# Optimization experiments

Hardware: AMD Instinct MI355X
Metric: run time of the kernel (lower is better)

Reference implementation:

```python
import jax, jax.numpy as jnp
import numpy as np

T = 8192   # sequence length (sent_len)
D = 512    # word_emb_dim
H = 2048   # enc_lstm_dim
S = 512    # number of segments (len(action_pos))
EPS = 1e-4 # additive constant in the original _masked_softmax denominator


def setup_inputs() -> dict:
    key = jax.random.key(0)
    ks = jax.random.split(key, 16)
    s = 0.02  # small init scale keeps exp() stable
    seg_len = T // S
    action_pos = (jnp.arange(1, S + 1, dtype=jnp.int32) * seg_len - 1)  # last = T-1
    action = jnp.zeros((T,), jnp.int32).at[action_pos].set(1)
    return {
        "sent": jax.random.normal(ks[0], (T, D), jnp.float32),
        "Wi1": jax.random.normal(ks[1], (3 * H, D), jnp.float32) * s,
        "Wh1": jax.random.normal(ks[2], (3 * H, H), jnp.float32) * s,
        "bi1": jax.random.normal(ks[3], (3 * H,), jnp.float32) * s,
        "bh1": jax.random.normal(ks[4], (3 * H,), jnp.float32) * s,
        "Wi2": jax.random.normal(ks[5], (3 * H, H), jnp.float32) * s,
        "Wh2": jax.random.normal(ks[6], (3 * H, H), jnp.float32) * s,
        "bi2": jax.random.normal(ks[7], (3 * H,), jnp.float32) * s,
        "bh2": jax.random.normal(ks[8], (3 * H,), jnp.float32) * s,
        "Wl": jax.random.normal(ks[9], (H, H), jnp.float32) * s,
        "bl": jax.random.normal(ks[10], (H,), jnp.float32) * s,
        "wa": jax.random.normal(ks[11], (H,), jnp.float32) * s,
        "Wl2": jax.random.normal(ks[12], (H, H), jnp.float32) * s,
        "bl2": jax.random.normal(ks[13], (H,), jnp.float32) * s,
        "wa2": jax.random.normal(ks[14], (H,), jnp.float32) * s,
        "action": action,
        "action_pos": action_pos,
    }


def _gru_scan(xs, reset, Wi, Wh, bi, bh):
    """GRU over leading axis; hidden state zeroed after steps where reset==1.
    xs: (N, in), reset: (N,) int. Returns outputs (N, H)."""
    gi_all = xs @ Wi.T + bi  # (N, 3H) precompute input gates as one GEMM

    def step(h, inp):
        gi, a = inp
        gh = Wh @ h + bh
        r = jax.nn.sigmoid(gi[:H] + gh[:H])
        z = jax.nn.sigmoid(gi[H:2 * H] + gh[H:2 * H])
        n = jnp.tanh(gi[2 * H:] + r * gh[2 * H:])
        hn = (1.0 - z) * n + z * h
        h_next = jnp.where(a == 1, jnp.zeros_like(hn), hn)
        return h_next, hn

    h0 = jnp.zeros((H,), xs.dtype)
    _, outs = jax.lax.scan(step, h0, (gi_all, reset))
    return outs


def _degenerate_softmax(a):
    # Original sums exp over a size-1 axis: w = exp(a) / (exp(a) + 1e-4)
    e = jnp.exp(a)
    return e / (e + EPS)


def reference(sent, Wi1, Wh1, bi1, bh1, Wi2, Wh2, bi2, bh2,
              Wl, bl, wa, Wl2, bl2, wa2, action, action_pos):
    # lower GRU with per-step state reset
    outs = _gru_scan(sent, action, Wi1, Wh1, bi1, bh1)          # (T, H)
    emb_h = jnp.tanh(outs @ Wl.T + bl)                           # (T, H)
    w = _degenerate_softmax(emb_h @ wa)                          # (T,)
    weighted = w[:, None] * emb_h                                # (T, H)
    # segment i covers tokens (action_pos[i-1], action_pos[i]]
    seg_id = jnp.searchsorted(action_pos, jnp.arange(T), side='left')
    seg = jax.ops.segment_max(weighted, seg_id, num_segments=S)  # (S, H)
    # upper GRU over segment embeddings (no resets, zero init)
    outs2 = _gru_scan(seg, jnp.zeros((S,), jnp.int32), Wi2, Wh2, bi2, bh2)
    e2 = jnp.tanh(outs2 @ Wl2.T + bl2)                           # (S, H)
    w2 = _degenerate_softmax(e2 @ wa2)                           # (S,)
    emb = jnp.max(w2[:, None] * e2, axis=0, keepdims=True)       # (1, H)
    return emb
```

## Files before the change

kernel.cpp:

```cpp
#include <hip/hip_runtime.h>
#include <stdint.h>

typedef unsigned short u16;
typedef unsigned int u32;
typedef unsigned long long u64;
typedef __attribute__((ext_vector_type(4))) float f32x4;
typedef __attribute__((ext_vector_type(8))) short bf16x8;
typedef __attribute__((ext_vector_type(4))) u32 u32x4;

constexpr int kT = 8192;
constexpr int kD = 512;
constexpr int kH = 2048;
constexpr int kH3 = 6144;
constexpr int kS = 512;
constexpr int kSeg = 16;
constexpr int kNWG2 = 256;
constexpr int kREP = 4;

__device__ __forceinline__ float bf2f(u16 u) {
  union { float f; u32 u; } v; v.u = ((u32)u) << 16; return v.f;
}
__device__ __forceinline__ u16 f2bf(float f) {
  union { float f; u32 u; } v; v.f = f;
  u32 lsb = (v.u >> 16) & 1u;
  v.u += 0x7fffu + lsb;
  return (u16)(v.u >> 16);
}
__device__ __forceinline__ float bflo(u32 x) {
  union { float f; u32 u; } v; v.u = x << 16; return v.f;
}
__device__ __forceinline__ float bfhi(u32 x) {
  union { float f; u32 u; } v; v.u = x & 0xffff0000u; return v.f;
}
__device__ __forceinline__ float sigm(float x) { return 1.f / (1.f + expf(-x)); }

__device__ __forceinline__ void g2l16(const u16* g, u16* l) {
  __builtin_amdgcn_global_load_lds(
      (const __attribute__((address_space(1))) u32*)g,
      (__attribute__((address_space(3))) u32*)l, 16, 0, 0);
}

__device__ __forceinline__ u32x4 bypass_load16(const u32* p) {
  u32x4 v;
  asm volatile("global_load_dwordx4 %0, %1, off sc0 sc1\n\ts_waitcnt vmcnt(0)"
               : "=&v"(v) : "v"(p) : "memory");
  return v;
}
__device__ __forceinline__ void bypass_store16(u32* p, u32x4 v) {
  asm volatile("global_store_dwordx4 %0, %1, off sc0 sc1" :: "v"(p), "v"(v) : "memory");
}

__global__ void cvt_bf16(const float* __restrict__ in, u16* __restrict__ out, int n4) {
  int i = blockIdx.x * blockDim.x + threadIdx.x;
  if (i >= n4) return;
  const float4 v = *(const float4*)(in + (size_t)i * 4);
  uint2 o;
  o.x = (u32)f2bf(v.x) | ((u32)f2bf(v.y) << 16);
  o.y = (u32)f2bf(v.z) | ((u32)f2bf(v.w) << 16);
  *(uint2*)(out + (size_t)i * 4) = o;
}

template<int EPI>
__global__ __launch_bounds__(256)
void gemm_bt(const u16* __restrict__ A, int lda,
             const u16* __restrict__ B, int ldb,
             u16* __restrict__ Obf, const float* __restrict__ bias,
             int M, int N, int K)
{
  __shared__ u16 ls[4 * 16384];
  const int tid = threadIdx.x;
  const int w = tid >> 6, lane = tid & 63;
  const int wr = w >> 1, wc = w & 1;
  const int arow0 = blockIdx.y * 128;
  const int brow0 = blockIdx.x * 128;
  const int srow = w * 32 + (lane >> 3);
  const int scol = (lane & 7) * 8;
  const u16* gA = A + (size_t)(arow0 + srow) * lda + scol;
  const u16* gB = B + (size_t)(brow0 + srow) * ldb + scol;
  const int sb = w * 32 * 64;

  f32x4 acc[4][4];
#pragma unroll
  for (int m = 0; m < 4; ++m)
#pragma unroll
    for (int n = 0; n < 4; ++n) acc[m][n] = (f32x4)0.f;

  const int fr = lane & 15;
  const int kq = lane >> 4;
  const int nk = K >> 6;

  auto stage = [&](int buf, int kt) {
    u16* la = &ls[buf * 16384 + sb];
    u16* lb = &ls[buf * 16384 + 8192 + sb];
#pragma unroll
    for (int i = 0; i < 4; ++i) g2l16(gA + (size_t)i * 8 * lda + kt, la + i * 8 * 64);
#pragma unroll
    for (int i = 0; i < 4; ++i) g2l16(gB + (size_t)i * 8 * ldb + kt, lb + i * 8 * 64);
  };

  stage(0, 0);
  if (nk > 1) stage(1, 64);
  if (nk > 2) stage(2, 128);

  for (int i = 0; i < nk; ++i) {
    if (i + 2 < nk) asm volatile("s_waitcnt vmcnt(16)" ::: "memory");
    else            asm volatile("s_waitcnt vmcnt(0)" ::: "memory");
    __builtin_amdgcn_s_barrier();
    __builtin_amdgcn_sched_barrier(0);
    if (i + 3 < nk) stage((i + 3) & 3, (i + 3) * 64);
    const u16* lsA = &ls[(i & 3) * 16384];
    const u16* lsB = lsA + 8192;
#pragma unroll
    for (int kk = 0; kk < 2; ++kk) {
      bf16x8 af[4], bq[4];
#pragma unroll
      for (int m = 0; m < 4; ++m)
        af[m] = *(const bf16x8*)&lsA[(wr * 64 + m * 16 + fr) * 64 + kk * 32 + kq * 8];
#pragma unroll
      for (int n = 0; n < 4; ++n)
        bq[n] = *(const bf16x8*)&lsB[(wc * 64 + n * 16 + fr) * 64 + kk * 32 + kq * 8];
#pragma unroll
      for (int m = 0; m < 4; ++m)
#pragma unroll
        for (int n = 0; n < 4; ++n)
          acc[m][n] = __builtin_amdgcn_mfma_f32_16x16x32_bf16(af[m], bq[n], acc[m][n], 0, 0, 0);
    }
  }

#pragma unroll
  for (int m = 0; m < 4; ++m) {
#pragma unroll
    for (int n = 0; n < 4; ++n) {
      const int row0 = arow0 + wr * 64 + m * 16 + kq * 4;
      const int col = brow0 + wc * 64 + n * 16 + fr;
      if (EPI == 1) {
#pragma unroll
        for (int i = 0; i < 4; ++i)
          Obf[(size_t)(row0 + i) * N + col] = f2bf(acc[m][n][i]);
      } else {
        const float bv = bias[col];
#pragma unroll
        for (int i = 0; i < 4; ++i)
          Obf[(size_t)(row0 + i) * N + col] = f2bf(tanhf(acc[m][n][i] + bv));
      }
    }
  }
}

__global__ __launch_bounds__(256) void gru1_gates(
    const u32* __restrict__ gi32, int segStride, const u16* __restrict__ gh,
    const float* __restrict__ bi, const float* __restrict__ bh,
    u16* __restrict__ h_bf, u16* __restrict__ outs_bf, int t, int ghvalid)
{
  const int idx = blockIdx.x * 256 + threadIdx.x;
  const int seg = idx >> 10, jp = idx & 1023;
  const u32* gh32 = (const u32*)gh;
  const int gbase = seg * segStride;
  const int base = seg * 3072;
  const u32 gir = gi32[gbase + jp];
  const u32 giz = gi32[gbase + 1024 + jp];
  const u32 gin = gi32[gbase + 2048 + jp];
  u32 ghr = 0, ghz = 0, ghn = 0, hp = 0;
  if (ghvalid) {
    ghr = gh32[base + jp];
    ghz = gh32[base + 1024 + jp];
    ghn = gh32[base + 2048 + jp];
    hp = ((const u32*)h_bf)[seg * 1024 + jp];
  }
  const float2 bir = *(const float2*)&bi[2 * jp];
  const float2 biz = *(const float2*)&bi[kH + 2 * jp];
  const float2 bin = *(const float2*)&bi[2 * kH + 2 * jp];
  const float2 bhr = *(const float2*)&bh[2 * jp];
  const float2 bhz = *(const float2*)&bh[kH + 2 * jp];
  const float2 bhn = *(const float2*)&bh[2 * kH + 2 * jp];
  float hn[2];
#pragma unroll
  for (int e = 0; e < 2; ++e) {
    const float gr = e ? bfhi(gir) : bflo(gir), hr = e ? bfhi(ghr) : bflo(ghr);
    const float gz = e ? bfhi(giz) : bflo(giz), hz = e ? bfhi(ghz) : bflo(ghz);
    const float gn = e ? bfhi(gin) : bflo(gin), hh = e ? bfhi(ghn) : bflo(ghn);
    const float r = sigm(gr + (e ? bir.y : bir.x) + hr + (e ? bhr.y : bhr.x));
    const float z = sigm(gz + (e ? biz.y : biz.x) + hz + (e ? bhz.y : bhz.x));
    const float n = tanhf(gn + (e ? bin.y : bin.x) + r * (hh + (e ? bhn.y : bhn.x)));
    const float hprev = e ? bfhi(hp) : bflo(hp);
    hn[e] = (1.f - z) * n + z * hprev;
  }
  const u32 packed = (u32)f2bf(hn[0]) | ((u32)f2bf(hn[1]) << 16);
  ((u32*)h_bf)[seg * 1024 + jp] = packed;
  ((u32*)outs_bf)[(size_t)(seg * kSeg + t) * 1024 + jp] = packed;
}

__global__ __launch_bounds__(256) void seg_weight_max(
    const u16* __restrict__ embh, const float* __restrict__ wa,
    u16* __restrict__ seg_bf)
{
  __shared__ float wrow[16];
  const int s = blockIdx.x, tid = threadIdx.x;
  const int w = tid >> 6, lane = tid & 63;
#pragma unroll
  for (int rr = 0; rr < 4; ++rr) {
    const int r = w * 4 + rr;
    const u16* row = embh + ((size_t)s * kSeg + r) * kH;
    float p = 0.f;
#pragma unroll
    for (int k = 0; k < 32; ++k) {
      const int c = lane + 64 * k;
      p += bf2f(row[c]) * wa[c];
    }
#pragma unroll
    for (int off = 32; off; off >>= 1) p += __shfl_down(p, off, 64);
    if (lane == 0) { const float e = expf(p); wrow[r] = e / (e + 1e-4f); }
  }
  __syncthreads();
#pragma unroll
  for (int i = 0; i < 8; ++i) {
    const int c = tid + 256 * i;
    float m = -1e30f;
#pragma unroll
    for (int r = 0; r < 16; ++r)
      m = fmaxf(m, wrow[r] * bf2f(embh[((size_t)s * kSeg + r) * kH + c]));
    seg_bf[(size_t)s * kH + c] = f2bf(m);
  }
}

__global__ __launch_bounds__(512)
void gru2_persistent(const u16* __restrict__ Wh2bf, const u16* __restrict__ gi2b,
                     const float* __restrict__ bi2, const float* __restrict__ bh2,
                     u32* __restrict__ hx,
                     u16* __restrict__ outs2)
{
  __shared__ u32 hlb[2][1024];
  __shared__ float gil_all[512 * 24];
  __shared__ float rowsum[24];
  __shared__ u16 hnl[8];
  const int wg = blockIdx.x, tid = threadIdx.x;
  const int g0 = wg * 8;
  const int rep = wg & (kREP - 1);
  const int w = tid >> 6, lane = tid & 63;

  u32 w0[16], w1[16], w2r[16];
#pragma unroll
  for (int rr = 0; rr < 3; ++rr) {
    const int lr = w * 3 + rr;
    const int grow = (lr >> 3) * kH + g0 + (lr & 7);
    const u32* src = (const u32*)(Wh2bf + (size_t)grow * kH) + lane * 16;
#pragma unroll
    for (int i = 0; i < 16; ++i) {
      const u32 val = src[i];
      if (rr == 0) w0[i] = val;
      else if (rr == 1) w1[i] = val;
      else w2r[i] = val;
    }
  }
  for (int i = tid; i < 512 * 24; i += 512) {
    const int t = i / 24, idx = i - t * 24;
    gil_all[i] = bf2f(gi2b[(size_t)t * kH3 + (idx >> 3) * kH + g0 + (idx & 7)]);
  }
  float bir = 0, biz = 0, bin = 0, bhr = 0, bhz = 0, bhn = 0;
  if (tid < 8) {
    const int jj = g0 + tid;
    bir = bi2[jj]; biz = bi2[kH + jj]; bin = bi2[2 * kH + jj];
    bhr = bh2[jj]; bhz = bh2[kH + jj]; bhn = bh2[2 * kH + jj];
  }

  for (int t = 0; t < 512; ++t) {
    const int par = t & 1;
    const u32 want = (u32)t & 0xffffu;
    const u32* p = hx + ((size_t)par * kREP + rep) * 2048 + 4 * tid;
    u32x4 v = bypass_load16(p);
    for (;;) {
      const u32 bad = ((v.x ^ want) | (v.y ^ want) | (v.z ^ want) | (v.w ^ want)) & 0xffffu;
      if (!__any((int)bad)) break;
      if (bad) v = bypass_load16(p);
    }
    hlb[par][2 * tid]     = (v.x >> 16) | (v.y & 0xffff0000u);
    hlb[par][2 * tid + 1] = (v.z >> 16) | (v.w & 0xffff0000u);
    __syncthreads();
    const uint4* hp4 = (const uint4*)&hlb[par][0];
    float hf[32];
#pragma unroll
    for (int q = 0; q < 4; ++q) {
      const uint4 hv = hp4[lane * 4 + q];
      hf[8 * q + 0] = bflo(hv.x); hf[8 * q + 1] = bfhi(hv.x);
      hf[8 * q + 2] = bflo(hv.y); hf[8 * q + 3] = bfhi(hv.y);
      hf[8 * q + 4] = bflo(hv.z); hf[8 * q + 5] = bfhi(hv.z);
      hf[8 * q + 6] = bflo(hv.w); hf[8 * q + 7] = bfhi(hv.w);
    }
    float a0 = 0.f, a1 = 0.f, a2 = 0.f;
#pragma unroll
    for (int i = 0; i < 16; ++i) {
      a0 += bflo(w0[i]) * hf[2 * i] + bfhi(w0[i]) * hf[2 * i + 1];
      a1 += bflo(w1[i]) * hf[2 * i] + bfhi(w1[i]) * hf[2 * i + 1];
      a2 += bflo(w2r[i]) * hf[2 * i] + bfhi(w2r[i]) * hf[2 * i + 1];
    }
#pragma unroll
    for (int off = 32; off; off >>= 1) {
      a0 += __shfl_down(a0, off, 64);
      a1 += __shfl_down(a1, off, 64);
      a2 += __shfl_down(a2, off, 64);
    }
    if (lane == 0) {
      rowsum[w * 3 + 0] = a0;
      rowsum[w * 3 + 1] = a1;
      rowsum[w * 3 + 2] = a2;
    }
    __syncthreads();
    if (tid < 8) {
      const float r = sigm(gil_all[t * 24 + tid] + bir + rowsum[tid] + bhr);
      const float z = sigm(gil_all[t * 24 + 8 + tid] + biz + rowsum[8 + tid] + bhz);
      const float n = tanhf(gil_all[t * 24 + 16 + tid] + bin +
                            r * (rowsum[16 + tid] + bhn));
      const u32 hw = hlb[par][(g0 + tid) >> 1];
      const float hprev = (tid & 1) ? bfhi(hw) : bflo(hw);
      hnl[tid] = f2bf((1.f - z) * n + z * hprev);
    }
    if (tid < 2 * kREP) {
      const int orep = tid >> 1, half = tid & 1;
      const u32 tagv = (u32)(t + 1) & 0xffffu;
      u32x4 m;
      m.x = ((u32)hnl[half * 4 + 0] << 16) | tagv;
      m.y = ((u32)hnl[half * 4 + 1] << 16) | tagv;
      m.z = ((u32)hnl[half * 4 + 2] << 16) | tagv;
      m.w = ((u32)hnl[half * 4 + 3] << 16) | tagv;
      u32* q = hx + ((size_t)(1 - par) * kREP + orep) * 2048 + wg * 8 + half * 4;
      bypass_store16(q, m);
    }
    if (tid == 0)
      *(uint4*)&outs2[(size_t)t * kH + g0] = *(const uint4*)hnl;
  }
}

__global__ void calc_w2(const u16* __restrict__ e2, const float* __restrict__ wa2,
                        float* __restrict__ w2) {
  const int s = blockIdx.x, lane = threadIdx.x;
  float p = 0.f;
#pragma unroll
  for (int k = 0; k < 32; ++k) {
    const int c = lane + 64 * k;
    p += bf2f(e2[(size_t)s * kH + c]) * wa2[c];
  }
#pragma unroll
  for (int off = 32; off; off >>= 1) p += __shfl_down(p, off, 64);
  if (lane == 0) { const float e = expf(p); w2[s] = e / (e + 1e-4f); }
}

__global__ void final_max(const u16* __restrict__ e2, const float* __restrict__ w2,
                          float* __restrict__ out) {
  const int j = blockIdx.x * blockDim.x + threadIdx.x;
  float m = -1e30f;
  for (int s = 0; s < 512; ++s)
    m = fmaxf(m, w2[s] * bf2f(e2[(size_t)s * kH + j]));
  out[j] = m;
}

extern "C" void kernel_launch(void* const* d_in, const int* in_sizes, int n_in,
                              void* d_out, int out_size, void* d_ws, size_t ws_size,
                              hipStream_t stream)
{
  (void)in_sizes; (void)n_in; (void)out_size;
  const float* sent = (const float*)d_in[0];
  const float* Wi1f = (const float*)d_in[1];
  const float* Wh1f = (const float*)d_in[2];
  const float* bi1  = (const float*)d_in[3];
  const float* bh1  = (const float*)d_in[4];
  const float* Wi2f = (const float*)d_in[5];
  const float* Wh2f = (const float*)d_in[6];
  const float* bi2  = (const float*)d_in[7];
  const float* bh2  = (const float*)d_in[8];
  const float* Wlf  = (const float*)d_in[9];
  const float* bl   = (const float*)d_in[10];
  const float* wa   = (const float*)d_in[11];
  const float* Wl2f = (const float*)d_in[12];
  const float* bl2  = (const float*)d_in[13];
  const float* wa2  = (const float*)d_in[14];
  float* out = (float*)d_out;

  char* base = (char*)d_ws;
  size_t off = 0;
  auto alloc = [&](size_t b) { char* p = base + off; off += (b + 255) & ~(size_t)255; return p; };
  u16* sent_bf = (u16*)alloc((size_t)kT * kD * 2);
  u16* Wi1b    = (u16*)alloc((size_t)kH3 * kD * 2);
  u16* Wh1b    = (u16*)alloc((size_t)kH3 * kH * 2);
  u16* Wi2b    = (u16*)alloc((size_t)kH3 * kH * 2);
  u16* Wh2b    = (u16*)alloc((size_t)kH3 * kH * 2);
  u16* Wlb     = (u16*)alloc((size_t)kH * kH * 2);
  u16* Wl2b    = (u16*)alloc((size_t)kH * kH * 2);
  u16* gi_buf  = (u16*)alloc((size_t)kS * kH3 * 2);
  u16* gh_buf  = (u16*)alloc((size_t)kS * kH3 * 2);
  u16* h1b     = (u16*)alloc((size_t)kS * kH * 2);
  u16* outs_bf = (u16*)alloc((size_t)kT * kH * 2);
  u16* seg_bf  = (u16*)alloc((size_t)kS * kH * 2);
  u32* hx      = (u32*)alloc((size_t)2 * kREP * 2048 * 4);
  u16* outs2   = (u16*)alloc((size_t)kS * kH * 2);
  u16* e2b     = (u16*)alloc((size_t)kS * kH * 2);
  float* w2    = (float*)alloc(kS * 4);
  const size_t off_before_gi = off;
  u16* gi_all  = (u16*)alloc((size_t)kT * kH3 * 2);
  const bool fused_gi = (off <= ws_size);
  if (!fused_gi) off = off_before_gi;
  u16* embh = sent_bf;
  u16* gi2b = gi_buf;

  (void)hipMemsetAsync(hx, 0, (size_t)2 * kREP * 2048 * 4, stream);

  auto cvt = [&](const float* src, u16* dst, int n) {
    const int n4 = n / 4;
    cvt_bf16<<<dim3((n4 + 255) / 256), dim3(256), 0, stream>>>(src, dst, n4);
  };
  cvt(sent, sent_bf, kT * kD);
  cvt(Wi1f, Wi1b, kH3 * kD);
  cvt(Wh1f, Wh1b, kH3 * kH);
  cvt(Wi2f, Wi2b, kH3 * kH);
  cvt(Wlf, Wlb, kH * kH);
  cvt(Wl2f, Wl2b, kH * kH);
  cvt(Wh2f, Wh2b, kH3 * kH);

  if (fused_gi) {
    gemm_bt<1><<<dim3(kH3 / 128, kT / 128), dim3(256), 0, stream>>>(
        sent_bf, kD, Wi1b, kD, gi_all, nullptr, kT, kH3, kD);
  }
  for (int t = 0; t < kSeg; ++t) {
    if (t > 0) {
      gemm_bt<1><<<dim3(kH3 / 128, kS / 128), dim3(256), 0, stream>>>(
          h1b, kH, Wh1b, kH, gh_buf, nullptr, kS, kH3, kH);
    }
    const u32* gi32;
    int segStride;
    if (fused_gi) {
      gi32 = (const u32*)gi_all + (size_t)t * 3072;
      segStride = kSeg * 3072;
    } else {
      gemm_bt<1><<<dim3(kH3 / 128, kS / 128), dim3(256), 0, stream>>>(
          sent_bf + t * kD, kSeg * kD, Wi1b, kD, gi_buf, nullptr, kS, kH3, kD);
      gi32 = (const u32*)gi_buf;
      segStride = 3072;
    }
    gru1_gates<<<dim3(kS * kH / 512), dim3(256), 0, stream>>>(
        gi32, segStride, gh_buf, bi1, bh1, h1b, outs_bf, t, t > 0 ? 1 : 0);
  }
  gemm_bt<2><<<dim3(kH / 128, kT / 128), dim3(256), 0, stream>>>(
      outs_bf, kH, Wlb, kH, embh, bl, kT, kH, kH);
  seg_weight_max<<<dim3(kS), dim3(256), 0, stream>>>(embh, wa, seg_bf);
  gemm_bt<1><<<dim3(kH3 / 128, kS / 128), dim3(256), 0, stream>>>(
      seg_bf, kH, Wi2b, kH, gi2b, nullptr, kS, kH3, kH);
  gru2_persistent<<<dim3(kNWG2), dim3(512), 0, stream>>>(
      Wh2b, gi2b, bi2, bh2, hx, outs2);
  gemm_bt<2><<<dim3(kH / 128, kS / 128), dim3(256), 0, stream>>>(
      outs2, kH, Wl2b, kH, e2b, bl2, kS, kH, kH);
  calc_w2<<<dim3(kS), dim3(64), 0, stream>>>(e2b, wa2, w2);
  final_max<<<dim3(kH / 256), dim3(256), 0, stream>>>(e2b, w2, out);
}
```

Measured before the change: 2.510 ms.

## Assign one hidden unit per wave in GRU2 step to drop second barrier

Reorganizes the persistent upper-GRU kernel so each wave owns all three gate rows (r, z, n) of one hidden unit instead of three arbitrary rows. Each wave can then reduce its own dot products and apply the gate math in lane 0 directly, removing the rowsum shared buffer and the second __syncthreads per timestep. Each lane 0 now publishes its own tagged hidden word with four scalar bypass stores to the replicas, replacing the 16-byte vector stores done by a few threads. The weight slices are also laid out so LDS reads of h are contiguous per lane. The trade-off is more, smaller global stores per step.

```diff
diff --git a/kernel.cpp b/kernel.cpp
--- a/kernel.cpp
+++ b/kernel.cpp
@@ -46,8 +46,8 @@
                : "=&v"(v) : "v"(p) : "memory");
   return v;
 }
-__device__ __forceinline__ void bypass_store16(u32* p, u32x4 v) {
-  asm volatile("global_store_dwordx4 %0, %1, off sc0 sc1" :: "v"(p), "v"(v) : "memory");
+__device__ __forceinline__ void bypass_store4(u32* p, u32 v) {
+  asm volatile("global_store_dword %0, %1, off sc0 sc1" :: "v"(p), "v"(v) : "memory");
 }
 
 __global__ void cvt_bf16(const float* __restrict__ in, u16* __restrict__ out, int n4) {
@@ -231,37 +231,33 @@
 {
   __shared__ u32 hlb[2][1024];
   __shared__ float gil_all[512 * 24];
-  __shared__ float rowsum[24];
-  __shared__ u16 hnl[8];
   const int wg = blockIdx.x, tid = threadIdx.x;
   const int g0 = wg * 8;
   const int rep = wg & (kREP - 1);
   const int w = tid >> 6, lane = tid & 63;
-
-  u32 w0[16], w1[16], w2r[16];
-#pragma unroll
-  for (int rr = 0; rr < 3; ++rr) {
-    const int lr = w * 3 + rr;
-    const int grow = (lr >> 3) * kH + g0 + (lr & 7);
-    const u32* src = (const u32*)(Wh2bf + (size_t)grow * kH) + lane * 16;
-#pragma unroll
-    for (int i = 0; i < 16; ++i) {
-      const u32 val = src[i];
-      if (rr == 0) w0[i] = val;
-      else if (rr == 1) w1[i] = val;
-      else w2r[i] = val;
-    }
+  const int jj = g0 + w;
+
+  u32 wr_[16], wz_[16], wn_[16];
+  {
+    const u32* rr = (const u32*)(Wh2bf + (size_t)jj * kH);
+    const u32* rz = (const u32*)(Wh2bf + (size_t)(kH + jj) * kH);
+    const u32* rn = (const u32*)(Wh2bf + (size_t)(2 * kH + jj) * kH);
+#pragma unroll
+    for (int q = 0; q < 4; ++q)
+#pragma unroll
+      for (int i = 0; i < 4; ++i) {
+        const int idx = q * 256 + lane * 4 + i;
+        wr_[q * 4 + i] = rr[idx];
+        wz_[q * 4 + i] = rz[idx];
+        wn_[q * 4 + i] = rn[idx];
+      }
   }
   for (int i = tid; i < 512 * 24; i += 512) {
     const int t = i / 24, idx = i - t * 24;
     gil_all[i] = bf2f(gi2b[(size_t)t * kH3 + (idx >> 3) * kH + g0 + (idx & 7)]);
   }
-  float bir = 0, biz = 0, bin = 0, bhr = 0, bhz = 0, bhn = 0;
-  if (tid < 8) {
-    const int jj = g0 + tid;
-    bir = bi2[jj]; biz = bi2[kH + jj]; bin = bi2[2 * kH + jj];
-    bhr = bh2[jj]; bhz = bh2[kH + jj]; bhn = bh2[2 * kH + jj];
-  }
+  const float bir = bi2[jj], biz = bi2[kH + jj], bin = bi2[2 * kH + jj];
+  const float bhr = bh2[jj], bhz = bh2[kH + jj], bhn = bh2[2 * kH + jj];
 
   for (int t = 0; t < 512; ++t) {
     const int par = t & 1;
@@ -277,56 +273,39 @@
     hlb[par][2 * tid + 1] = (v.z >> 16) | (v.w & 0xffff0000u);
     __syncthreads();
     const uint4* hp4 = (const uint4*)&hlb[par][0];
-    float hf[32];
+    float ar = 0.f, az = 0.f, an = 0.f;
 #pragma unroll
     for (int q = 0; q < 4; ++q) {
-      const uint4 hv = hp4[lane * 4 + q];
-      hf[8 * q + 0] = bflo(hv.x); hf[8 * q + 1] = bfhi(hv.x);
-      hf[8 * q + 2] = bflo(hv.y); hf[8 * q + 3] = bfhi(hv.y);
-      hf[8 * q + 4] = bflo(hv.z); hf[8 * q + 5] = bfhi(hv.z);
-      hf[8 * q + 6] = bflo(hv.w); hf[8 * q + 7] = bfhi(hv.w);
-    }
-    float a0 = 0.f, a1 = 0.f, a2 = 0.f;
-#pragma unroll
-    for (int i = 0; i < 16; ++i) {
-      a0 += bflo(w0[i]) * hf[2 * i] + bfhi(w0[i]) * hf[2 * i + 1];
-      a1 += bflo(w1[i]) * hf[2 * i] + bfhi(w1[i]) * hf[2 * i + 1];
-      a2 += bflo(w2r[i]) * hf[2 * i] + bfhi(w2r[i]) * hf[2 * i + 1];
+      const uint4 hv = hp4[q * 64 + lane];
+      const float hf[8] = { bflo(hv.x), bfhi(hv.x), bflo(hv.y), bfhi(hv.y),
+                            bflo(hv.z), bfhi(hv.z), bflo(hv.w), bfhi(hv.w) };
+#pragma unroll
+      for (int i = 0; i < 4; ++i) {
+        const u32 wrv = wr_[q * 4 + i], wzv = wz_[q * 4 + i], wnv = wn_[q * 4 + i];
+        ar += bflo(wrv) * hf[2 * i] + bfhi(wrv) * hf[2 * i + 1];
+        az += bflo(wzv) * hf[2 * i] + bfhi(wzv) * hf[2 * i + 1];
+        an += bflo(wnv) * hf[2 * i] + bfhi(wnv) * hf[2 * i + 1];
+      }
     }
 #pragma unroll
     for (int off = 32; off; off >>= 1) {
-      a0 += __shfl_down(a0, off, 64);
-      a1 += __shfl_down(a1, off, 64);
-      a2 += __shfl_down(a2, off, 64);
+      ar += __shfl_down(ar, off, 64);
+      az += __shfl_down(az, off, 64);
+      an += __shfl_down(an, off, 64);
     }
     if (lane == 0) {
-      rowsum[w * 3 + 0] = a0;
-      rowsum[w * 3 + 1] = a1;
-      rowsum[w * 3 + 2] = a2;
-    }
-    __syncthreads();
-    if (tid < 8) {
-      const float r = sigm(gil_all[t * 24 + tid] + bir + rowsum[tid] + bhr);
-      const float z = sigm(gil_all[t * 24 + 8 + tid] + biz + rowsum[8 + tid] + bhz);
-      const float n = tanhf(gil_all[t * 24 + 16 + tid] + bin +
-                            r * (rowsum[16 + tid] + bhn));
-      const u32 hw = hlb[par][(g0 + tid) >> 1];
-      const float hprev = (tid & 1) ? bfhi(hw) : bflo(hw);
-      hnl[tid] = f2bf((1.f - z) * n + z * hprev);
-    }
-    if (tid < 2 * kREP) {
-      const int orep = tid >> 1, half = tid & 1;
-      const u32 tagv = (u32)(t + 1) & 0xffffu;
-      u32x4 m;
-      m.x = ((u32)hnl[half * 4 + 0] << 16) | tagv;
-      m.y = ((u32)hnl[half * 4 + 1] << 16) | tagv;
-      m.z = ((u32)hnl[half * 4 + 2] << 16) | tagv;
-      m.w = ((u32)hnl[half * 4 + 3] << 16) | tagv;
-      u32* q = hx + ((size_t)(1 - par) * kREP + orep) * 2048 + wg * 8 + half * 4;
-      bypass_store16(q, m);
-    }
-    if (tid == 0)
-      *(uint4*)&outs2[(size_t)t * kH + g0] = *(const uint4*)hnl;
+      const float r = sigm(gil_all[t * 24 + w] + bir + ar + bhr);
+      const float z = sigm(gil_all[t * 24 + 8 + w] + biz + az + bhz);
+      const float n = tanhf(gil_all[t * 24 + 16 + w] + bin + r * (an + bhn));
+      const u32 hw = hlb[par][jj >> 1];
+      const float hprev = (jj & 1) ? bfhi(hw) : bflo(hw);
+      const u16 hb = f2bf((1.f - z) * n + z * hprev);
+      const u32 word = ((u32)hb << 16) | ((u32)(t + 1) & 0xffffu);
+#pragma unroll
+      for (int orep = 0; orep < kREP; ++orep)
+        bypass_store4(hx + ((size_t)(1 - par) * kREP + orep) * 2048 + jj, word);
+      outs2[(size_t)t * kH + jj] = hb;
+    }
   }
 }
 
```

After: 3.139 ms. +25.1%, slower.
